# Kernel tuning notes

Measured on AMD Instinct MI355X. Metric: run time of the kernel, lower is better.

## Reference

```python
import jax, jax.numpy as jnp
import numpy as np


def setup_inputs() -> dict:
    key = jax.random.key(0)
    ks = jax.random.split(key, 16)
    B, T, H = 64, 512, 256
    s = lambda n: 1.0 / np.sqrt(n)
    return {
        "q_vec": jax.random.normal(ks[0], (B, H), jnp.float32),
        "fact_vecs": jax.random.normal(ks[1], (B, T, H), jnp.float32),
        "input_len": jax.random.randint(ks[2], (B,), 1, T + 1, jnp.int32),
        "W1": jax.random.normal(ks[3], (7 * H, H), jnp.float32) * s(7 * H),
        "b1": jnp.zeros((H,), jnp.float32),
        "W2": jax.random.normal(ks[4], (H, 1), jnp.float32) * s(H),
        "b2": jnp.zeros((1,), jnp.float32),
        "Wr": jax.random.normal(ks[5], (H, H), jnp.float32) * s(H),
        "Ur": jax.random.normal(ks[6], (H, H), jnp.float32) * s(H),
        "br": jnp.zeros((H,), jnp.float32),
        "Wh": jax.random.normal(ks[7], (H, H), jnp.float32) * s(H),
        "Uh": jax.random.normal(ks[8], (H, H), jnp.float32) * s(H),
        "bh": jnp.zeros((H,), jnp.float32),
        "Ws": jax.random.normal(ks[9], (2 * H, 1), jnp.float32) * s(2 * H),
        "bs": jnp.zeros((1,), jnp.float32),
        "We": jax.random.normal(ks[10], (2 * H, 1), jnp.float32) * s(2 * H),
        "be": jnp.zeros((1,), jnp.float32),
    }


def reference(q_vec, fact_vecs, input_len, W1, b1, W2, b2,
              Wr, Ur, br, Wh, Uh, bh, Ws, bs, We, be):
    B, T, H = fact_vecs.shape
    m = q_vec  # prev_memory = q_vec (never actually updated in the original inference loop)
    qb = jnp.broadcast_to(q_vec[:, None, :], (B, T, H))
    mb = qb  # m == q_vec
    f = fact_vecs
    # episodic attention features: [f, m, q, f*q, f*m, |f-q|, |f-m|] -> [B,T,7H]
    feats = jnp.concatenate(
        [f, mb, qb, f * qb, f * mb, jnp.abs(f - qb), jnp.abs(f - mb)], axis=-1)
    att = jnp.tanh(feats @ W1 + b1) @ W2 + b2          # [B,T,1]
    g = jax.nn.softmax(att[..., 0], axis=1)            # [B,T]

    # AttentionGRU scan over time with sequence-length masking (dynamic_rnn semantics)
    valid = (jnp.arange(T)[:, None] < input_len[None, :])  # [T,B]

    def step(h, inp):
        x_t, g_t, v_t = inp  # [B,H], [B], [B]
        r = jax.nn.sigmoid(x_t @ Wr + h @ Ur + br)
        hc = jnp.tanh(x_t @ Wh + (r * h) @ Uh + bh)
        hn = g_t[:, None] * hc + (1.0 - g_t[:, None]) * h
        hn = jnp.where(v_t[:, None], hn, h)
        out = jnp.where(v_t[:, None], hn, jnp.zeros_like(hn))
        return hn, out

    xs = (jnp.swapaxes(fact_vecs, 0, 1), g.T, valid)
    _, outs = jax.lax.scan(step, jnp.zeros((B, H), fact_vecs.dtype), xs)
    e_outputs = jnp.swapaxes(outs, 0, 1)               # [B,T,H]

    # predict_position (final hop, is_iteration=False): tanh dense over [prev_memory, e_t]
    cat = jnp.concatenate([jnp.broadcast_to(m[:, None, :], (B, T, H)), e_outputs], axis=-1)
    out_s = jnp.tanh(cat @ Ws + bs)[..., 0]            # [B,T]
    out_e = jnp.tanh(cat @ We + be)[..., 0]            # [B,T]
    return out_s, out_e
```

## Files before the change

kernel.cpp:

```cpp
#include <hip/hip_runtime.h>
#include <cstddef>


static __device__ __forceinline__ float b2f(unsigned short u) {
  return __uint_as_float(((unsigned)u) << 16);
}
static __device__ __forceinline__ float blo(unsigned w) { return __uint_as_float(w << 16); }
static __device__ __forceinline__ float bhi(unsigned w) { return __uint_as_float(w & 0xffff0000u); }
static __device__ __forceinline__ unsigned short f2b(float f) {
  unsigned u = __float_as_uint(f);
  u += 0x7fffu + ((u >> 16) & 1u);
  return (unsigned short)(u >> 16);
}
static __device__ __forceinline__ float ldf(const void* b, size_t i, int md) {
  return md ? ((const float*)b)[i] : b2f(((const unsigned short*)b)[i]);
}
static __device__ __forceinline__ unsigned short ldb(const void* b, size_t i, int md) {
  return md ? f2b(((const float*)b)[i]) : ((const unsigned short*)b)[i];
}

typedef short bfrag __attribute__((ext_vector_type(8)));
typedef float f32x4 __attribute__((ext_vector_type(4)));

template <int CTRL>
static __device__ __forceinline__ float dpp_add(float x) {
  int v = __builtin_amdgcn_update_dpp(0, __float_as_int(x), CTRL, 0xF, 0xF, true);
  return x + __int_as_float(v);
}
static __device__ __forceinline__ float red16(float x) {
  x = dpp_add<0xB1>(x);
  x = dpp_add<0x4E>(x);
  x = dpp_add<0x141>(x);
  x = dpp_add<0x140>(x);
  return x;
}
static __device__ __forceinline__ void sync_lds() {
  __builtin_amdgcn_fence(__ATOMIC_RELEASE, "workgroup", "local");
  __builtin_amdgcn_s_barrier();
  __builtin_amdgcn_fence(__ATOMIC_ACQUIRE, "workgroup", "local");
}
static __device__ __forceinline__ float fast_tanh(float x) {
  float xc = fminf(fmaxf(x, -15.f), 15.f);
  return 1.f - 2.f * __builtin_amdgcn_rcpf(__expf(2.f * xc) + 1.f);
}

__global__ void k_detect(const void* __restrict__ fact, int* __restrict__ mode) {
  int tid = threadIdx.x;
  const unsigned short* u = (const unsigned short*)fact;
  float v = fabsf(b2f(u[2 * tid]));
  if (!(v == v)) v = 1e30f;
  for (int o = 32; o > 0; o >>= 1) v = fmaxf(v, __shfl_xor(v, o));
  __shared__ float red[4];
  int wave = tid >> 6, lane = tid & 63;
  if (lane == 0) red[wave] = v;
  __syncthreads();
  if (tid == 0) {
    float m = fmaxf(fmaxf(red[0], red[1]), fmaxf(red[2], red[3]));
    mode[0] = (m > 1e4f) ? 1 : 0;
  }
}

__global__ void k_prep_w(const void* __restrict__ W1,
                         const void* __restrict__ Wr,
                         const void* __restrict__ Wh,
                         const void* __restrict__ Ur,
                         const void* __restrict__ Uh,
                         const int* __restrict__ mode,
                         unsigned* __restrict__ W5q,
                         unsigned* __restrict__ Urp,
                         unsigned* __restrict__ Uhp) {
  int md = *mode;
  int idx = blockIdx.x * 256 + threadIdx.x;
  int i = idx >> 8, j = idx & 255;
  Urp[idx] = (unsigned)ldb(Ur, (size_t)(2 * i) * 256 + j, md) |
             ((unsigned)ldb(Ur, (size_t)(2 * i + 1) * 256 + j, md) << 16);
  Uhp[idx] = (unsigned)ldb(Uh, (size_t)(2 * i) * 256 + j, md) |
             ((unsigned)ldb(Uh, (size_t)(2 * i + 1) * 256 + j, md) << 16);
  float v0, v1;
  int p;
  p = i;
  v0 = ldf(W1, (size_t)(2 * i) * 256 + j, md);
  v1 = ldf(W1, (size_t)(2 * i + 1) * 256 + j, md);
  W5q[(((p >> 2) * 256 + j) << 2) + (p & 3)] = (unsigned)f2b(v0) | ((unsigned)f2b(v1) << 16);
  p = 128 + i;
  v0 = ldf(W1, (size_t)(768 + 2 * i) * 256 + j, md) + ldf(W1, (size_t)(1024 + 2 * i) * 256 + j, md);
  v1 = ldf(W1, (size_t)(769 + 2 * i) * 256 + j, md) + ldf(W1, (size_t)(1025 + 2 * i) * 256 + j, md);
  W5q[(((p >> 2) * 256 + j) << 2) + (p & 3)] = (unsigned)f2b(v0) | ((unsigned)f2b(v1) << 16);
  p = 256 + i;
  v0 = ldf(W1, (size_t)(1280 + 2 * i) * 256 + j, md) + ldf(W1, (size_t)(1536 + 2 * i) * 256 + j, md);
  v1 = ldf(W1, (size_t)(1281 + 2 * i) * 256 + j, md) + ldf(W1, (size_t)(1537 + 2 * i) * 256 + j, md);
  W5q[(((p >> 2) * 256 + j) << 2) + (p & 3)] = (unsigned)f2b(v0) | ((unsigned)f2b(v1) << 16);
  p = 384 + i;
  v0 = ldf(Wr, (size_t)(2 * i) * 256 + j, md);
  v1 = ldf(Wr, (size_t)(2 * i + 1) * 256 + j, md);
  W5q[(((p >> 2) * 256 + j) << 2) + (p & 3)] = (unsigned)f2b(v0) | ((unsigned)f2b(v1) << 16);
  p = 512 + i;
  v0 = ldf(Wh, (size_t)(2 * i) * 256 + j, md);
  v1 = ldf(Wh, (size_t)(2 * i + 1) * 256 + j, md);
  W5q[(((p >> 2) * 256 + j) << 2) + (p & 3)] = (unsigned)f2b(v0) | ((unsigned)f2b(v1) << 16);
}

__global__ void k_prep_q(const void* __restrict__ q,
                         const void* __restrict__ W1,
                         const void* __restrict__ b1,
                         const void* __restrict__ Ws,
                         const void* __restrict__ bs,
                         const void* __restrict__ We,
                         const void* __restrict__ be,
                         const int* __restrict__ mode,
                         float* __restrict__ qw1,
                         float* __restrict__ qs,
                         float* __restrict__ qe) {
  __shared__ float qsh[256];
  __shared__ float reds[4], rede[4];
  int md = *mode;
  int b = blockIdx.x, tid = threadIdx.x;
  float qv = ldf(q, (size_t)b * 256 + tid, md);
  qsh[tid] = qv;
  __syncthreads();
  float acc = ldf(b1, tid, md);
  for (int i = 0; i < 256; ++i) {
    float w = ldf(W1, (size_t)(256 + i) * 256 + tid, md) + ldf(W1, (size_t)(512 + i) * 256 + tid, md);
    acc = fmaf(qsh[i], w, acc);
  }
  qw1[b * 256 + tid] = acc;
  float ps = qv * ldf(Ws, tid, md);
  float pe = qv * ldf(We, tid, md);
  for (int o = 32; o > 0; o >>= 1) { ps += __shfl_down(ps, o); pe += __shfl_down(pe, o); }
  int wave = tid >> 6, lane = tid & 63;
  if (lane == 0) { reds[wave] = ps; rede[wave] = pe; }
  __syncthreads();
  if (tid == 0) {
    qs[b] = ldf(bs, 0, md) + reds[0] + reds[1] + reds[2] + reds[3];
    qe[b] = ldf(be, 0, md) + rede[0] + rede[1] + rede[2] + rede[3];
  }
}

__launch_bounds__(256, 2)
__global__ void k_main(const void* __restrict__ fact,
                       const void* __restrict__ q,
                       const unsigned* __restrict__ W5q,
                       const float* __restrict__ qw1,
                       const void* __restrict__ W2,
                       const void* __restrict__ b2v,
                       const void* __restrict__ br,
                       const void* __restrict__ bh,
                       const int* __restrict__ mode,
                       float* __restrict__ att,
                       unsigned* __restrict__ xrh) {
  __shared__ __align__(16) unsigned short A[16 * 776];
  __shared__ float wsc[64];
  int md = *mode;
  int blk = blockIdx.x;
  int b = blk >> 5, t0 = (blk & 31) * 16;
  int tid = threadIdx.x;
  {
    float qv = ldf(q, (size_t)b * 256 + tid, md);
    for (int r = 0; r < 16; ++r) {
      float f = ldf(fact, ((size_t)(b * 512 + t0 + r)) * 256 + tid, md);
      A[r * 776 + tid] = f2b(f);
      A[r * 776 + 256 + tid] = f2b(f * qv);
      A[r * 776 + 512 + tid] = f2b(fabsf(f - qv));
    }
  }
  __syncthreads();
  int wv = tid >> 6, lane = tid & 63;
  int n16 = lane & 15, quad = lane >> 4;
  int colb = wv * 64 + n16;
  const uint4* W4 = (const uint4*)W5q;
  f32x4 z = {0.f, 0.f, 0.f, 0.f};
  f32x4 u[4] = {z, z, z, z}, ar[4] = {z, z, z, z}, ah[4] = {z, z, z, z};
#pragma unroll
  for (int kc = 0; kc < 8; ++kc) {
    uint4 av = *(const uint4*)((const char*)A + n16 * 1552 + kc * 64 + quad * 16);
    bfrag af = __builtin_bit_cast(bfrag, av);
    int pg = kc * 4 + quad;
#pragma unroll
    for (int tile = 0; tile < 4; ++tile) {
      int col = colb + tile * 16;
      uint4 bu = W4[(size_t)pg * 256 + col];
      uint4 bw = W4[(size_t)(96 + pg) * 256 + col];
      uint4 bv = W4[(size_t)(128 + pg) * 256 + col];
      u[tile] = __builtin_amdgcn_mfma_f32_16x16x32_bf16(af, __builtin_bit_cast(bfrag, bu), u[tile], 0, 0, 0);
      ar[tile] = __builtin_amdgcn_mfma_f32_16x16x32_bf16(af, __builtin_bit_cast(bfrag, bw), ar[tile], 0, 0, 0);
      ah[tile] = __builtin_amdgcn_mfma_f32_16x16x32_bf16(af, __builtin_bit_cast(bfrag, bv), ah[tile], 0, 0, 0);
    }
  }
#pragma unroll
  for (int kc = 8; kc < 24; ++kc) {
    uint4 av = *(const uint4*)((const char*)A + n16 * 1552 + kc * 64 + quad * 16);
    bfrag af = __builtin_bit_cast(bfrag, av);
    int pg = kc * 4 + quad;
#pragma unroll
    for (int tile = 0; tile < 4; ++tile) {
      int col = colb + tile * 16;
      uint4 bu = W4[(size_t)pg * 256 + col];
      u[tile] = __builtin_amdgcn_mfma_f32_16x16x32_bf16(af, __builtin_bit_cast(bfrag, bu), u[tile], 0, 0, 0);
    }
  }
  float qwv[4], w2v[4], brv[4], bhv[4];
#pragma unroll
  for (int tile = 0; tile < 4; ++tile) {
    int col = colb + tile * 16;
    qwv[tile] = qw1[b * 256 + col];
    w2v[tile] = ldf(W2, col, md);
    brv[tile] = ldf(br, col, md);
    bhv[tile] = ldf(bh, col, md);
  }
  float ps[4];
#pragma unroll
  for (int reg = 0; reg < 4; ++reg) {
    float p = 0.f;
#pragma unroll
    for (int tile = 0; tile < 4; ++tile) {
      float hid = fast_tanh(u[tile][reg] + qwv[tile]);
      p = fmaf(hid, w2v[tile], p);
    }
    ps[reg] = red16(p);
  }
  if (n16 == 0) {
#pragma unroll
    for (int reg = 0; reg < 4; ++reg) wsc[wv * 16 + quad * 4 + reg] = ps[reg];
  }
  __syncthreads();
  if (tid < 16) {
    att[b * 512 + t0 + tid] =
        wsc[tid] + wsc[16 + tid] + wsc[32 + tid] + wsc[48 + tid] + ldf(b2v, 0, md);
  }
#pragma unroll
  for (int tile = 0; tile < 4; ++tile) {
    int col = colb + tile * 16;
#pragma unroll
    for (int reg = 0; reg < 4; ++reg) {
      int t = t0 + quad * 4 + reg;
      unsigned v = (unsigned)f2b(ar[tile][reg] + brv[tile]) |
                   ((unsigned)f2b(ah[tile][reg] + bhv[tile]) << 16);
      xrh[((size_t)(b * 512 + t)) * 256 + col] = v;
    }
  }
}

__global__ void k_softmax(const float* __restrict__ att, float* __restrict__ g) {
  __shared__ float red[8];
  int b = blockIdx.x, tid = threadIdx.x;
  float v = att[b * 512 + tid];
  float m = v;
  for (int o = 32; o > 0; o >>= 1) m = fmaxf(m, __shfl_xor(m, o));
  int wave = tid >> 6, lane = tid & 63;
  if (lane == 0) red[wave] = m;
  __syncthreads();
  m = red[0];
#pragma unroll
  for (int w = 1; w < 8; ++w) m = fmaxf(m, red[w]);
  float e = __expf(v - m);
  float s = e;
  for (int o = 32; o > 0; o >>= 1) s += __shfl_xor(s, o);
  __syncthreads();
  if (lane == 0) red[wave] = s;
  __syncthreads();
  s = red[0] + red[1] + red[2] + red[3] + red[4] + red[5] + red[6] + red[7];
  g[b * 512 + tid] = e / s;
}

__launch_bounds__(512, 2)
__global__ void k_scan(const unsigned* __restrict__ Urp,
                       const unsigned* __restrict__ Uhp,
                       const unsigned* __restrict__ xrh,
                       const float* __restrict__ g,
                       const int* __restrict__ input_len,
                       const void* __restrict__ Ws,
                       const void* __restrict__ We,
                       const float* __restrict__ qs,
                       const float* __restrict__ qe,
                       const int* __restrict__ mode,
                       float* __restrict__ out) {
  __shared__ __align__(16) unsigned short hB[4 * 272];
  __shared__ __align__(16) unsigned short rhB[4 * 272];
  __shared__ float sacc[4][512];
  __shared__ float eacc[4][512];
  int md = *mode;
  int b0 = blockIdx.x * 4;
  int tid = threadIdx.x;
  int wv = tid >> 6, lane = tid & 63;
  int n16 = lane & 15, quad = lane >> 4;
  int col0 = wv * 32 + n16;
  int col1 = col0 + 16;
  uint4 br4[2][8], bh4[2][8];
#pragma unroll
  for (int tile = 0; tile < 2; ++tile) {
    int col = wv * 32 + tile * 16 + n16;
#pragma unroll
    for (int kc = 0; kc < 8; ++kc) {
      int p = kc * 16 + quad * 4;
      uint4 rv = {Urp[(size_t)p * 256 + col], Urp[(size_t)(p + 1) * 256 + col],
                  Urp[(size_t)(p + 2) * 256 + col], Urp[(size_t)(p + 3) * 256 + col]};
      uint4 hv = {Uhp[(size_t)p * 256 + col], Uhp[(size_t)(p + 1) * 256 + col],
                  Uhp[(size_t)(p + 2) * 256 + col], Uhp[(size_t)(p + 3) * 256 + col]};
      br4[tile][kc] = rv;
      bh4[tile][kc] = hv;
    }
  }
  for (int i = tid; i < 4 * 272; i += 512) { hB[i] = 0; rhB[i] = 0; }
  for (int i = tid; i < 2048; i += 512) { ((float*)sacc)[i] = 0.f; ((float*)eacc)[i] = 0.f; }
  int mylen = input_len[b0 + quad];
  float ws0 = ldf(Ws, 256 + col0, md), ws1 = ldf(Ws, 256 + col1, md);
  float we0 = ldf(We, 256 + col0, md), we1 = ldf(We, 256 + col1, md);
  float hm0 = 0.f, hm1 = 0.f;
  const char* hbase = (const char*)hB + (n16 >> 2) * 544 + quad * 16;
  const char* rhbase = (const char*)rhB + (n16 >> 2) * 544 + quad * 16;
  const unsigned* xrow = xrh + (size_t)(b0 + quad) * 512 * 256;
  const float* grow = g + (size_t)(b0 + quad) * 512;

  unsigned xa[16], xbb[16];
  float4 ga0, ga1, gb0, gb1;
  auto prefetch = [&](int tb, unsigned (&xr)[16], float4& g0, float4& g1) {
    const unsigned* xp = xrow + (size_t)tb * 8 * 256;
#pragma unroll
    for (int s = 0; s < 8; ++s) {
      xr[2 * s] = xp[s * 256 + col0];
      xr[2 * s + 1] = xp[s * 256 + col1];
    }
    const float* gp = grow + tb * 8;
    g0 = *(const float4*)gp;
    g1 = *(const float4*)(gp + 4);
  };
  prefetch(0, xa, ga0, ga1);
  __syncthreads();
  const f32x4 z4 = {0.f, 0.f, 0.f, 0.f};

  auto step = [&](int T, unsigned XC0, unsigned XC1, float GT) {
    f32x4 accA[2][4];
#pragma unroll
    for (int tl = 0; tl < 2; ++tl)
#pragma unroll
      for (int j = 0; j < 4; ++j) accA[tl][j] = z4;
#pragma unroll
    for (int kc = 0; kc < 8; ++kc) {
      uint4 av = *(const uint4*)(hbase + kc * 64);
      bfrag af = __builtin_bit_cast(bfrag, av);
      int j = kc & 3;
      accA[0][j] = __builtin_amdgcn_mfma_f32_16x16x32_bf16(af, __builtin_bit_cast(bfrag, br4[0][kc]), accA[0][j], 0, 0, 0);
      accA[1][j] = __builtin_amdgcn_mfma_f32_16x16x32_bf16(af, __builtin_bit_cast(bfrag, br4[1][kc]), accA[1][j], 0, 0, 0);
    }
    {
      float v0 = (accA[0][0][0] + accA[0][1][0]) + (accA[0][2][0] + accA[0][3][0]);
      float v1 = (accA[1][0][0] + accA[1][1][0]) + (accA[1][2][0] + accA[1][3][0]);
      float e0 = __expf(-(v0 + blo(XC0)));
      float e1 = __expf(-(v1 + blo(XC1)));
      float r0 = __builtin_amdgcn_rcpf(1.f + e0);
      float r1 = __builtin_amdgcn_rcpf(1.f + e1);
      rhB[quad * 272 + col0] = f2b(r0 * hm0);
      rhB[quad * 272 + col1] = f2b(r1 * hm1);
    }
    sync_lds();
    f32x4 accB[2][4];
#pragma unroll
    for (int tl = 0; tl < 2; ++tl)
#pragma unroll
      for (int j = 0; j < 4; ++j) accB[tl][j] = z4;
#pragma unroll
    for (int kc = 0; kc < 8; ++kc) {
      uint4 av = *(const uint4*)(rhbase + kc * 64);
      bfrag af = __builtin_bit_cast(bfrag, av);
      int j = kc & 3;
      accB[0][j] = __builtin_amdgcn_mfma_f32_16x16x32_bf16(af, __builtin_bit_cast(bfrag, bh4[0][kc]), accB[0][j], 0, 0, 0);
      accB[1][j] = __builtin_amdgcn_mfma_f32_16x16x32_bf16(af, __builtin_bit_cast(bfrag, bh4[1][kc]), accB[1][j], 0, 0, 0);
    }
    {
      float w0 = (accB[0][0][0] + accB[0][1][0]) + (accB[0][2][0] + accB[0][3][0]);
      float w1 = (accB[1][0][0] + accB[1][1][0]) + (accB[1][2][0] + accB[1][3][0]);
      float c0 = fminf(fmaxf(w0 + bhi(XC0), -15.f), 15.f);
      float c1 = fminf(fmaxf(w1 + bhi(XC1), -15.f), 15.f);
      float hc0 = 1.f - 2.f * __builtin_amdgcn_rcpf(__expf(2.f * c0) + 1.f);
      float hc1 = 1.f - 2.f * __builtin_amdgcn_rcpf(__expf(2.f * c1) + 1.f);
      bool valid = T < mylen;
      float hn0 = hm0 + GT * (hc0 - hm0);
      float hn1 = hm1 + GT * (hc1 - hm1);
      hm0 = valid ? hn0 : hm0;
      hm1 = valid ? hn1 : hm1;
      hB[quad * 272 + col0] = f2b(hm0);
      hB[quad * 272 + col1] = f2b(hm1);
      float p_s = valid ? fmaf(hm0, ws0, hm1 * ws1) : 0.f;
      float p_e = valid ? fmaf(hm0, we0, hm1 * we1) : 0.f;
      p_s = red16(p_s);
      p_e = red16(p_e);
      if (n16 == 0) {
        atomicAdd(&sacc[quad][T], p_s);
        atomicAdd(&eacc[quad][T], p_e);
      }
    }
    sync_lds();
  };

  for (int tb2 = 0; tb2 < 32; ++tb2) {
    prefetch(2 * tb2 + 1, xbb, gb0, gb1);
#pragma unroll
    for (int tt = 0; tt < 8; ++tt)
      step(tb2 * 16 + tt, xa[2 * tt], xa[2 * tt + 1], tt < 4 ? ga0[tt] : ga1[tt - 4]);
    prefetch(tb2 < 31 ? 2 * tb2 + 2 : 63, xa, ga0, ga1);
#pragma unroll
    for (int tt = 0; tt < 8; ++tt)
      step(tb2 * 16 + 8 + tt, xbb[2 * tt], xbb[2 * tt + 1], tt < 4 ? gb0[tt] : gb1[tt - 4]);
  }
  sync_lds();
  for (int i = tid; i < 2048; i += 512) {
    int b = i >> 9, t = i & 511;
    int row = (b0 + b) * 512 + t;
    out[row] = tanhf(qs[b0 + b] + sacc[b][t]);
    out[32768 + row] = tanhf(qe[b0 + b] + eacc[b][t]);
  }
}

extern "C" void kernel_launch(void* const* d_in, const int* in_sizes, int n_in,
                              void* d_out, int out_size, void* d_ws, size_t ws_size,
                              hipStream_t stream) {
  const void* q    = d_in[0];
  const void* fact = d_in[1];
  const int* ilen  = (const int*)d_in[2];
  const void* W1   = d_in[3];
  const void* b1   = d_in[4];
  const void* W2   = d_in[5];
  const void* b2v  = d_in[6];
  const void* Wr   = d_in[7];
  const void* Ur   = d_in[8];
  const void* br   = d_in[9];
  const void* Wh   = d_in[10];
  const void* Uh   = d_in[11];
  const void* bh   = d_in[12];
  const void* Ws   = d_in[13];
  const void* bs   = d_in[14];
  const void* We   = d_in[15];
  const void* be   = d_in[16];

  char* w = (char*)d_ws;
  unsigned* W5q = (unsigned*)(w);
  unsigned* Urp = (unsigned*)(w + 1310720);
  unsigned* Uhp = (unsigned*)(w + 1441792);
  float*    qw1 = (float*)(w + 1572864);
  float*    qs  = (float*)(w + 1638400);
  float*    qe  = (float*)(w + 1638656);
  float*    att = (float*)(w + 1638912);
  float*    g   = (float*)(w + 1769984);
  unsigned* xrh = (unsigned*)(w + 1901056);
  int*      mode = (int*)(w + 52232704);
  float* out = (float*)d_out;

  k_detect<<<dim3(1), dim3(256), 0, stream>>>(fact, mode);
  k_prep_w<<<dim3(128), dim3(256), 0, stream>>>(W1, Wr, Wh, Ur, Uh, mode, W5q, Urp, Uhp);
  k_prep_q<<<dim3(64), dim3(256), 0, stream>>>(q, W1, b1, Ws, bs, We, be, mode, qw1, qs, qe);
  k_main<<<dim3(2048), dim3(256), 0, stream>>>(fact, q, W5q, qw1, W2, b2v, br, bh, mode, att, xrh);
  k_softmax<<<dim3(64), dim3(512), 0, stream>>>(att, g);
  k_scan<<<dim3(16), dim3(512), 0, stream>>>(Urp, Uhp, xrh, g, ilen, Ws, We, qs, qe, mode, out);
}
```

Baseline: 689.4 us.

## Double k_main row tile for weight reuse and defer scan output reduction

k_main now handles 32 time rows per block instead of 16, so each weight fragment loaded from global memory feeds two MFMAs and the grid halves. This cuts W1/Wr/Wh traffic per row, at the cost of more accumulator registers and twice the LDS footprint, which may lower occupancy. Separately, the scan kernel defers the Ws/We projection reduction and its atomics by one step. That work now runs while the next step's first MFMA batch completes, taking it off the serial critical path between the two LDS syncs.

```diff
diff --git a/kernel.cpp b/kernel.cpp
--- a/kernel.cpp
+++ b/kernel.cpp
@@ -148,15 +148,15 @@
                        const int* __restrict__ mode,
                        float* __restrict__ att,
                        unsigned* __restrict__ xrh) {
-  __shared__ __align__(16) unsigned short A[16 * 776];
-  __shared__ float wsc[64];
+  __shared__ __align__(16) unsigned short A[32 * 776];
+  __shared__ float wsc[128];
   int md = *mode;
   int blk = blockIdx.x;
-  int b = blk >> 5, t0 = (blk & 31) * 16;
+  int b = blk >> 4, t0 = (blk & 15) * 32;
   int tid = threadIdx.x;
   {
     float qv = ldf(q, (size_t)b * 256 + tid, md);
-    for (int r = 0; r < 16; ++r) {
+    for (int r = 0; r < 32; ++r) {
       float f = ldf(fact, ((size_t)(b * 512 + t0 + r)) * 256 + tid, md);
       A[r * 776 + tid] = f2b(f);
       A[r * 776 + 256 + tid] = f2b(f * qv);
@@ -169,11 +169,17 @@
   int colb = wv * 64 + n16;
   const uint4* W4 = (const uint4*)W5q;
   f32x4 z = {0.f, 0.f, 0.f, 0.f};
-  f32x4 u[4] = {z, z, z, z}, ar[4] = {z, z, z, z}, ah[4] = {z, z, z, z};
+  f32x4 u[2][4], ar[2][4], ah[2][4];
+#pragma unroll
+  for (int rt = 0; rt < 2; ++rt)
+#pragma unroll
+    for (int tile = 0; tile < 4; ++tile) { u[rt][tile] = z; ar[rt][tile] = z; ah[rt][tile] = z; }
 #pragma unroll
   for (int kc = 0; kc < 8; ++kc) {
-    uint4 av = *(const uint4*)((const char*)A + n16 * 1552 + kc * 64 + quad * 16);
-    bfrag af = __builtin_bit_cast(bfrag, av);
+    uint4 av0 = *(const uint4*)((const char*)A + n16 * 1552 + kc * 64 + quad * 16);
+    uint4 av1 = *(const uint4*)((const char*)A + (16 + n16) * 1552 + kc * 64 + quad * 16);
+    bfrag af0 = __builtin_bit_cast(bfrag, av0);
+    bfrag af1 = __builtin_bit_cast(bfrag, av1);
     int pg = kc * 4 + quad;
 #pragma unroll
     for (int tile = 0; tile < 4; ++tile) {
@@ -181,21 +187,31 @@
       uint4 bu = W4[(size_t)pg * 256 + col];
       uint4 bw = W4[(size_t)(96 + pg) * 256 + col];
       uint4 bv = W4[(size_t)(128 + pg) * 256 + col];
-      u[tile] = __builtin_amdgcn_mfma_f32_16x16x32_bf16(af, __builtin_bit_cast(bfrag, bu), u[tile], 0, 0, 0);
-      ar[tile] = __builtin_amdgcn_mfma_f32_16x16x32_bf16(af, __builtin_bit_cast(bfrag, bw), ar[tile], 0, 0, 0);
-      ah[tile] = __builtin_amdgcn_mfma_f32_16x16x32_bf16(af, __builtin_bit_cast(bfrag, bv), ah[tile], 0, 0, 0);
+      bfrag bfu = __builtin_bit_cast(bfrag, bu);
+      bfrag bfw = __builtin_bit_cast(bfrag, bw);
+      bfrag bfv = __builtin_bit_cast(bfrag, bv);
+      u[0][tile] = __builtin_amdgcn_mfma_f32_16x16x32_bf16(af0, bfu, u[0][tile], 0, 0, 0);
+      u[1][tile] = __builtin_amdgcn_mfma_f32_16x16x32_bf16(af1, bfu, u[1][tile], 0, 0, 0);
+      ar[0][tile] = __builtin_amdgcn_mfma_f32_16x16x32_bf16(af0, bfw, ar[0][tile], 0, 0, 0);
+      ar[1][tile] = __builtin_amdgcn_mfma_f32_16x16x32_bf16(af1, bfw, ar[1][tile], 0, 0, 0);
+      ah[0][tile] = __builtin_amdgcn_mfma_f32_16x16x32_bf16(af0, bfv, ah[0][tile], 0, 0, 0);
+      ah[1][tile] = __builtin_amdgcn_mfma_f32_16x16x32_bf16(af1, bfv, ah[1][tile], 0, 0, 0);
     }
   }
 #pragma unroll
   for (int kc = 8; kc < 24; ++kc) {
-    uint4 av = *(const uint4*)((const char*)A + n16 * 1552 + kc * 64 + quad * 16);
-    bfrag af = __builtin_bit_cast(bfrag, av);
+    uint4 av0 = *(const uint4*)((const char*)A + n16 * 1552 + kc * 64 + quad * 16);
+    uint4 av1 = *(const uint4*)((const char*)A + (16 + n16) * 1552 + kc * 64 + quad * 16);
+    bfrag af0 = __builtin_bit_cast(bfrag, av0);
+    bfrag af1 = __builtin_bit_cast(bfrag, av1);
     int pg = kc * 4 + quad;
 #pragma unroll
     for (int tile = 0; tile < 4; ++tile) {
       int col = colb + tile * 16;
       uint4 bu = W4[(size_t)pg * 256 + col];
-      u[tile] = __builtin_amdgcn_mfma_f32_16x16x32_bf16(af, __builtin_bit_cast(bfrag, bu), u[tile], 0, 0, 0);
+      bfrag bfu = __builtin_bit_cast(bfrag, bu);
+      u[0][tile] = __builtin_amdgcn_mfma_f32_16x16x32_bf16(af0, bfu, u[0][tile], 0, 0, 0);
+      u[1][tile] = __builtin_amdgcn_mfma_f32_16x16x32_bf16(af1, bfu, u[1][tile], 0, 0, 0);
     }
   }
   float qwv[4], w2v[4], brv[4], bhv[4];
@@ -207,37 +223,45 @@
     brv[tile] = ldf(br, col, md);
     bhv[tile] = ldf(bh, col, md);
   }
-  float ps[4];
-#pragma unroll
-  for (int reg = 0; reg < 4; ++reg) {
-    float p = 0.f;
+  float ps[2][4];
+#pragma unroll
+  for (int rt = 0; rt < 2; ++rt)
+#pragma unroll
+    for (int reg = 0; reg < 4; ++reg) {
+      float p = 0.f;
+#pragma unroll
+      for (int tile = 0; tile < 4; ++tile) {
+        float hid = fast_tanh(u[rt][tile][reg] + qwv[tile]);
+        p = fmaf(hid, w2v[tile], p);
+      }
+      ps[rt][reg] = red16(p);
+    }
+  if (n16 == 0) {
+#pragma unroll
+    for (int rt = 0; rt < 2; ++rt)
+#pragma unroll
+      for (int reg = 0; reg < 4; ++reg) wsc[rt * 64 + wv * 16 + quad * 4 + reg] = ps[rt][reg];
+  }
+  __syncthreads();
+  if (tid < 32) {
+    int rt = tid >> 4, tl = tid & 15;
+    att[b * 512 + t0 + rt * 16 + tl] =
+        wsc[rt * 64 + tl] + wsc[rt * 64 + 16 + tl] + wsc[rt * 64 + 32 + tl] + wsc[rt * 64 + 48 + tl] +
+        ldf(b2v, 0, md);
+  }
+#pragma unroll
+  for (int rt = 0; rt < 2; ++rt)
 #pragma unroll
     for (int tile = 0; tile < 4; ++tile) {
-      float hid = fast_tanh(u[tile][reg] + qwv[tile]);
-      p = fmaf(hid, w2v[tile], p);
-    }
-    ps[reg] = red16(p);
-  }
-  if (n16 == 0) {
-#pragma unroll
-    for (int reg = 0; reg < 4; ++reg) wsc[wv * 16 + quad * 4 + reg] = ps[reg];
-  }
-  __syncthreads();
-  if (tid < 16) {
-    att[b * 512 + t0 + tid] =
-        wsc[tid] + wsc[16 + tid] + wsc[32 + tid] + wsc[48 + tid] + ldf(b2v, 0, md);
-  }
-#pragma unroll
-  for (int tile = 0; tile < 4; ++tile) {
-    int col = colb + tile * 16;
-#pragma unroll
-    for (int reg = 0; reg < 4; ++reg) {
-      int t = t0 + quad * 4 + reg;
-      unsigned v = (unsigned)f2b(ar[tile][reg] + brv[tile]) |
-                   ((unsigned)f2b(ah[tile][reg] + bhv[tile]) << 16);
-      xrh[((size_t)(b * 512 + t)) * 256 + col] = v;
-    }
-  }
+      int col = colb + tile * 16;
+#pragma unroll
+      for (int reg = 0; reg < 4; ++reg) {
+        int t = t0 + rt * 16 + quad * 4 + reg;
+        unsigned v = (unsigned)f2b(ar[rt][tile][reg] + brv[tile]) |
+                     ((unsigned)f2b(ah[rt][tile][reg] + bhv[tile]) << 16);
+        xrh[((size_t)(b * 512 + t)) * 256 + col] = v;
+      }
+    }
 }
 
 __global__ void k_softmax(const float* __restrict__ att, float* __restrict__ g) {
@@ -306,6 +330,8 @@
   float ws0 = ldf(Ws, 256 + col0, md), ws1 = ldf(Ws, 256 + col1, md);
   float we0 = ldf(We, 256 + col0, md), we1 = ldf(We, 256 + col1, md);
   float hm0 = 0.f, hm1 = 0.f;
+  float pend_s = 0.f, pend_e = 0.f;
+  int pend_T = 0;
   const char* hbase = (const char*)hB + (n16 >> 2) * 544 + quad * 16;
   const char* rhbase = (const char*)rhB + (n16 >> 2) * 544 + quad * 16;
   const unsigned* xrow = xrh + (size_t)(b0 + quad) * 512 * 256;
@@ -341,6 +367,14 @@
       int j = kc & 3;
       accA[0][j] = __builtin_amdgcn_mfma_f32_16x16x32_bf16(af, __builtin_bit_cast(bfrag, br4[0][kc]), accA[0][j], 0, 0, 0);
       accA[1][j] = __builtin_amdgcn_mfma_f32_16x16x32_bf16(af, __builtin_bit_cast(bfrag, br4[1][kc]), accA[1][j], 0, 0, 0);
+    }
+    {
+      float rs = red16(pend_s);
+      float re_ = red16(pend_e);
+      if (n16 == 0) {
+        atomicAdd(&sacc[quad][pend_T], rs);
+        atomicAdd(&eacc[quad][pend_T], re_);
+      }
     }
     {
       float v0 = (accA[0][0][0] + accA[0][1][0]) + (accA[0][2][0] + accA[0][3][0]);
@@ -380,14 +414,9 @@
       hm1 = valid ? hn1 : hm1;
       hB[quad * 272 + col0] = f2b(hm0);
       hB[quad * 272 + col1] = f2b(hm1);
-      float p_s = valid ? fmaf(hm0, ws0, hm1 * ws1) : 0.f;
-      float p_e = valid ? fmaf(hm0, we0, hm1 * we1) : 0.f;
-      p_s = red16(p_s);
-      p_e = red16(p_e);
-      if (n16 == 0) {
-        atomicAdd(&sacc[quad][T], p_s);
-        atomicAdd(&eacc[quad][T], p_e);
-      }
+      pend_s = valid ? fmaf(hm0, ws0, hm1 * ws1) : 0.f;
+      pend_e = valid ? fmaf(hm0, we0, hm1 * we1) : 0.f;
+      pend_T = T;
     }
     sync_lds();
   };
@@ -401,6 +430,14 @@
 #pragma unroll
     for (int tt = 0; tt < 8; ++tt)
       step(tb2 * 16 + 8 + tt, xbb[2 * tt], xbb[2 * tt + 1], tt < 4 ? gb0[tt] : gb1[tt - 4]);
+  }
+  {
+    float rs = red16(pend_s);
+    float re_ = red16(pend_e);
+    if (n16 == 0) {
+      atomicAdd(&sacc[quad][pend_T], rs);
+      atomicAdd(&eacc[quad][pend_T], re_);
+    }
   }
   sync_lds();
   for (int i = tid; i < 2048; i += 512) {
@@ -448,7 +485,7 @@
   k_detect<<<dim3(1), dim3(256), 0, stream>>>(fact, mode);
   k_prep_w<<<dim3(128), dim3(256), 0, stream>>>(W1, Wr, Wh, Ur, Uh, mode, W5q, Urp, Uhp);
   k_prep_q<<<dim3(64), dim3(256), 0, stream>>>(q, W1, b1, Ws, bs, We, be, mode, qw1, qs, qe);
-  k_main<<<dim3(2048), dim3(256), 0, stream>>>(fact, q, W5q, qw1, W2, b2v, br, bh, mode, att, xrh);
+  k_main<<<dim3(1024), dim3(256), 0, stream>>>(fact, q, W5q, qw1, W2, b2v, br, bh, mode, att, xrh);
   k_softmax<<<dim3(64), dim3(512), 0, stream>>>(att, g);
   k_scan<<<dim3(16), dim3(512), 0, stream>>>(Urp, Uhp, xrh, g, ilen, Ws, We, qs, qe, mode, out);
 }
```

Measured after the change: 659.1 us. -4.4%, faster.
